# Kernel optimization log

Hardware: AMD Instinct MI355X
Metric: run time of the kernel (lower is better)

Reference implementation:

```python
import jax, jax.numpy as jnp
import numpy as np

NH = 8      # num_heads
KP = 3      # propagation_steps

def _ln(x, g, b, eps=1e-5):
    m = jnp.mean(x, -1, keepdims=True)
    v = jnp.mean(jnp.square(x - m), -1, keepdims=True)
    return (x - m) * jax.lax.rsqrt(v + eps) * g + b

def _mha(x, Wq, bq, Wk, bk, Wv, bv, Wo, bo):
    B, L, H = x.shape
    dh = H // NH
    q = (x @ Wq + bq).reshape(B, L, NH, dh)
    k = (x @ Wk + bk).reshape(B, L, NH, dh)
    v = (x @ Wv + bv).reshape(B, L, NH, dh)
    s = jnp.einsum('blhd,bmhd->bhlm', q, k) / jnp.sqrt(jnp.asarray(dh, x.dtype))
    p = jax.nn.softmax(s, axis=-1)
    o = jnp.einsum('bhlm,bmhd->blhd', p, v).reshape(B, L, H)
    return o @ Wo + bo

def setup_inputs():
    B, S, N, H = 2, 12, 800, 64
    keys = jax.random.split(jax.random.key(0), 64)
    it = iter(range(64))
    def nk():
        return keys[next(it)]
    def w(shape):
        return jax.random.normal(nk(), shape, jnp.float32) * 0.02
    p = {}
    p['x'] = jax.random.normal(nk(), (B, S, N, H), jnp.float32)
    # uniform weights scaled by 1/N (~row-normalized dense adjacency)
    p['adj'] = jax.random.uniform(nk(), (B, N, N), jnp.float32) / N
    p['W_gp'] = w((H, H)); p['b_gp'] = jnp.zeros((H,), jnp.float32)
    for sfx in ('s', 't'):
        for nm in ('Wq', 'Wk', 'Wv', 'Wo'):
            p[nm + '_' + sfx] = w((H, H))
        for nm in ('bq', 'bk', 'bv', 'bo'):
            p[nm + '_' + sfx] = jnp.zeros((H,), jnp.float32)
        p['g_' + sfx] = jnp.ones((H,), jnp.float32)
        p['be_' + sfx] = jnp.zeros((H,), jnp.float32)
    p['W1'] = w((H, 4 * H)); p['b1'] = jnp.zeros((4 * H,), jnp.float32)
    p['W2'] = w((4 * H, H)); p['b2'] = jnp.zeros((H,), jnp.float32)
    p['g1'] = jnp.ones((H,), jnp.float32); p['be1'] = jnp.zeros((H,), jnp.float32)
    p['g2'] = jnp.ones((H,), jnp.float32); p['be2'] = jnp.zeros((H,), jnp.float32)
    return p

def reference(x, adj, W_gp, b_gp,
              Wq_s, Wk_s, Wv_s, Wo_s, bq_s, bk_s, bv_s, bo_s, g_s, be_s,
              Wq_t, Wk_t, Wv_t, Wo_t, bq_t, bk_t, bv_t, bo_t, g_t, be_t,
              W1, b1, W2, b2, g1, be1, g2, be2):
    B, S, N, H = x.shape
    residual = x
    # accident-aware scaling (hidden_dim >= 6 path)
    acc = x[..., -2] * jnp.exp(-x[..., -1] / 60.0)
    xs = x * (1.0 + 0.3 * acc[..., None])
    # graph propagation: linear then K steps of relu(A @ h), vectorized over time
    h = xs @ W_gp + b_gp
    for _ in range(KP):
        h = jax.nn.relu(jnp.einsum('bnm,bsmh->bsnh', adj, h))
    prop = h + residual
    # spatial attention over nodes within each timestep
    xsa = prop.reshape(B * S, N, H)
    a = _mha(xsa, Wq_s, bq_s, Wk_s, bk_s, Wv_s, bv_s, Wo_s, bo_s)
    a = _ln(a + xsa, g_s, be_s).reshape(B, S, N, H)
    # temporal attention over timesteps per node
    xta = a.transpose(0, 2, 1, 3).reshape(B * N, S, H)
    t = _mha(xta, Wq_t, bq_t, Wk_t, bk_t, Wv_t, bv_t, Wo_t, bo_t)
    t = _ln(t + xta, g_t, be_t).reshape(B, N, S, H).transpose(0, 2, 1, 3)
    attn_out = t
    # pre-norm FFN with residual, post-norm output
    f = _ln(attn_out, g1, be1)
    f = jax.nn.relu(f @ W1 + b1) @ W2 + b2
    f = f + attn_out
    return _ln(f, g2, be2)
```

## Files before the change

### kernel.cpp

```cpp
#include <hip/hip_runtime.h>
#include <hip/hip_bf16.h>

#define NB 2
#define NS 12
#define NN 800
#define HEADS 8
#define DH 8
#define NBS (NB*NS)
#define NR (NB*NS*NN)

typedef __attribute__((ext_vector_type(4))) float f32x4;
typedef __attribute__((ext_vector_type(4))) short s16x4;
typedef __attribute__((ext_vector_type(8))) short s16x8;

static __device__ __forceinline__ unsigned short f2bf(float f) {
  union { float f; unsigned u; } v; v.f = f;
  unsigned r = (v.u + 0x7FFFu + ((v.u >> 16) & 1u)) >> 16;
  return (unsigned short)r;
}
static __device__ __forceinline__ float bf2f(unsigned short u) {
  union { unsigned u; float f; } v;
  v.u = ((unsigned)u) << 16;
  return v.f;
}
static __device__ __forceinline__ float fexp2(float x) {
  return __builtin_amdgcn_exp2f(x);
}
static __device__ __forceinline__ unsigned cvtpk_bf16(float a, float b) {
  unsigned r;
  asm("v_cvt_pk_bf16_f32 %0, %1, %2" : "=v"(r) : "v"(a), "v"(b));
  return r;
}

#define SC_LOG2 (0.35355339059327373f * 1.44269504088896f)

__global__ __launch_bounds__(256) void k_adjbf(const float* __restrict__ adj,
                                               unsigned short* __restrict__ o) {
  int i = blockIdx.x * 256 + threadIdx.x;
  if (i >= NB * NN * NN / 4) return;
  float4 a = *(const float4*)(adj + (size_t)i * 4);
  ushort4 r;
  r.x = f2bf(a.x); r.y = f2bf(a.y); r.z = f2bf(a.z); r.w = f2bf(a.w);
  *(ushort4*)(o + (size_t)i * 4) = r;
}

__global__ __launch_bounds__(256) void k_w2bf(
    const float* __restrict__ w0, const float* __restrict__ w1,
    const float* __restrict__ w2, const float* __restrict__ w3,
    const float* __restrict__ w4, const float* __restrict__ w5,
    const float* __restrict__ w6, const float* __restrict__ w7,
    const float* __restrict__ w8, unsigned short* __restrict__ out) {
  const float* ws[9] = {w0, w1, w2, w3, w4, w5, w6, w7, w8};
  int y = blockIdx.y;
  int i = blockIdx.x * 256 + threadIdx.x;
  if (i < 4096) out[y * 4096 + i] = f2bf(ws[y][i]);
}

__global__ __launch_bounds__(256) void k_f2bf(const float* __restrict__ src,
                                              unsigned short* __restrict__ dst,
                                              int n) {
  int i = blockIdx.x * 256 + threadIdx.x;
  if (i < n) dst[i] = f2bf(src[i]);
}

__global__ __launch_bounds__(256) void k_lin64T(
    const float* __restrict__ x, const unsigned short* __restrict__ Wb,
    const float* __restrict__ bias, unsigned short* __restrict__ HP) {
  __shared__ unsigned short As[32][36];
  __shared__ unsigned short Bs[64][36];
  const int tid = threadIdx.x;
  const int r0 = blockIdx.x * 32;
  const int w = tid >> 6, l = tid & 63;
  const int rb = (w & 1) * 16, cb = (w >> 1) * 32;
  f32x4 acc0 = {0.f, 0.f, 0.f, 0.f}, acc1 = {0.f, 0.f, 0.f, 0.f};
  const int ar = tid >> 3, ak = (tid & 7) * 4;
  const int bc = tid & 63, bm0 = (tid >> 6) * 4;
  const int k4 = (l >> 4) * 4;
  const int arow = rb + (l & 15);
  const int bcol0 = cb + (l & 15);
  const float* xrow = x + (size_t)(r0 + ar) * 64;
  float sf = 1.0f + 0.3f * xrow[62] * __expf(-xrow[63] * (1.0f / 60.0f));
  for (int k0 = 0; k0 < 64; k0 += 32) {
    __syncthreads();
    float4 xv = *(const float4*)(xrow + k0 + ak);
    ushort4 xb;
    xb.x = f2bf(xv.x * sf); xb.y = f2bf(xv.y * sf);
    xb.z = f2bf(xv.z * sf); xb.w = f2bf(xv.w * sf);
    *(ushort4*)&As[ar][ak] = xb;
#pragma unroll
    for (int j = 0; j < 4; ++j) {
      int mp = bm0 + j;
      unsigned lo = Wb[(size_t)(k0 + 2 * mp) * 64 + bc];
      unsigned hi = Wb[(size_t)(k0 + 2 * mp + 1) * 64 + bc];
      *(unsigned*)&Bs[bc][2 * mp] = lo | (hi << 16);
    }
    __syncthreads();
    s16x4 alo = *(const s16x4*)&As[arow][k4];
    s16x4 ahi = *(const s16x4*)&As[arow][k4 + 16];
    s16x8 a = {alo.x, alo.y, alo.z, alo.w, ahi.x, ahi.y, ahi.z, ahi.w};
    s16x4 b0l = *(const s16x4*)&Bs[bcol0][k4];
    s16x4 b0h = *(const s16x4*)&Bs[bcol0][k4 + 16];
    s16x8 bf0 = {b0l.x, b0l.y, b0l.z, b0l.w, b0h.x, b0h.y, b0h.z, b0h.w};
    s16x4 b1l = *(const s16x4*)&Bs[bcol0 + 16][k4];
    s16x4 b1h = *(const s16x4*)&Bs[bcol0 + 16][k4 + 16];
    s16x8 bf1 = {b1l.x, b1l.y, b1l.z, b1l.w, b1h.x, b1h.y, b1h.z, b1h.w};
    acc0 = __builtin_amdgcn_mfma_f32_16x16x32_bf16(a, bf0, acc0, 0, 0, 0);
    acc1 = __builtin_amdgcn_mfma_f32_16x16x32_bf16(a, bf1, acc1, 0, 0, 0);
  }
  const int c0 = cb + (l & 15);
  float b0 = bias[c0], b1 = bias[c0 + 16];
#pragma unroll
  for (int r = 0; r < 4; ++r) {
    int row = r0 + rb + (l >> 4) * 4 + r;
    int bs = row / NN, m = row % NN;
    HP[((size_t)bs * 64 + c0) * NN + m] = f2bf(acc0[r] + b0);
    HP[((size_t)bs * 64 + c0 + 16) * NN + m] = f2bf(acc1[r] + b1);
  }
}

template <bool LAST>
__global__ __launch_bounds__(256) void k_prop_mfma(
    const unsigned short* __restrict__ adjB,
    const unsigned short* __restrict__ HPin,
    const float* __restrict__ x,
    unsigned short* __restrict__ HPout,
    float* __restrict__ pout,
    unsigned short* __restrict__ pbout) {
  __shared__ unsigned short As[32][36];
  __shared__ unsigned short Bs[64][40];
  const int tid = threadIdx.x;
  const int bid = blockIdx.x;
  const int bs = bid / 25, mt = bid % 25;
  const int b = bs / NS;
  const int n0 = mt * 32;
  const unsigned short* abase = adjB + (size_t)b * NN * NN + (size_t)n0 * NN;
  const unsigned short* hbase = HPin + (size_t)bs * 64 * NN;
  const int w = tid >> 6, l = tid & 63;
  const int rb = (w & 1) * 16;
  const int cb = (w >> 1) * 32;
  f32x4 acc0 = {0.f, 0.f, 0.f, 0.f}, acc1 = {0.f, 0.f, 0.f, 0.f};
  const int ar = tid >> 3, ak = (tid & 7) * 4;
  const int bc = tid & 63, bq = tid >> 6;
  const int k4 = (l >> 4) * 4;
  const int arow = rb + (l & 15);
  const int bcol0 = cb + (l & 15);
  for (int m0 = 0; m0 < NN; m0 += 32) {
    __syncthreads();
    *(s16x4*)&As[ar][ak] = *(const s16x4*)(abase + (size_t)ar * NN + m0 + ak);
    *(s16x8*)&Bs[bc][bq * 8] =
        *(const s16x8*)(hbase + (size_t)bc * NN + m0 + bq * 8);
    __syncthreads();
    s16x4 alo = *(const s16x4*)&As[arow][k4];
    s16x4 ahi = *(const s16x4*)&As[arow][k4 + 16];
    s16x8 a = {alo.x, alo.y, alo.z, alo.w, ahi.x, ahi.y, ahi.z, ahi.w};
    s16x4 b0l = *(const s16x4*)&Bs[bcol0][k4];
    s16x4 b0h = *(const s16x4*)&Bs[bcol0][k4 + 16];
    s16x8 bf0 = {b0l.x, b0l.y, b0l.z, b0l.w, b0h.x, b0h.y, b0h.z, b0h.w};
    s16x4 b1l = *(const s16x4*)&Bs[bcol0 + 16][k4];
    s16x4 b1h = *(const s16x4*)&Bs[bcol0 + 16][k4 + 16];
    s16x8 bf1 = {b1l.x, b1l.y, b1l.z, b1l.w, b1h.x, b1h.y, b1h.z, b1h.w};
    acc0 = __builtin_amdgcn_mfma_f32_16x16x32_bf16(a, bf0, acc0, 0, 0, 0);
    acc1 = __builtin_amdgcn_mfma_f32_16x16x32_bf16(a, bf1, acc1, 0, 0, 0);
  }
  const int c0 = cb + (l & 15);
  if (LAST) {
#pragma unroll
    for (int r = 0; r < 4; ++r) {
      int n = n0 + rb + (l >> 4) * 4 + r;
      float v0 = fmaxf(acc0[r], 0.f);
      float v1 = fmaxf(acc1[r], 0.f);
      size_t i0 = ((size_t)bs * NN + n) * 64 + c0;
      size_t i1 = i0 + 16;
      float p0 = v0 + x[i0], p1 = v1 + x[i1];
      pout[i0] = p0;
      pout[i1] = p1;
      pbout[i0] = f2bf(p0);
      pbout[i1] = f2bf(p1);
    }
  } else {
    int nb = n0 + rb + (l >> 4) * 4;
    s16x4 o0, o1;
#pragma unroll
    for (int r = 0; r < 4; ++r) {
      o0[r] = (short)f2bf(fmaxf(acc0[r], 0.f));
      o1[r] = (short)f2bf(fmaxf(acc1[r], 0.f));
    }
    *(s16x4*)&HPout[((size_t)bs * 64 + c0) * NN + nb] = o0;
    *(s16x4*)&HPout[((size_t)bs * 64 + c0 + 16) * NN + nb] = o1;
  }
}

__global__ __launch_bounds__(256) void k_qkv_mfma(
    const unsigned short* __restrict__ Xb,
    const unsigned short* __restrict__ Wq,
    const unsigned short* __restrict__ Wk,
    const unsigned short* __restrict__ Wv,
    const float* __restrict__ bq, const float* __restrict__ bk,
    const float* __restrict__ bv, float qscale,
    unsigned short* __restrict__ Qo, unsigned short* __restrict__ Ko,
    unsigned short* __restrict__ Vo) {
  __shared__ unsigned short As[32][36];
  __shared__ unsigned short Bs[3][64][36];
  const int tid = threadIdx.x;
  const int r0 = blockIdx.x * 32;
  const int w = tid >> 6, l = tid & 63;
  const int rb = (w & 1) * 16;
  const int cb = (w >> 1) * 32;
  f32x4 acc[3][2];
#pragma unroll
  for (int i = 0; i < 3; ++i)
#pragma unroll
    for (int j = 0; j < 2; ++j) acc[i][j] = (f32x4){0.f, 0.f, 0.f, 0.f};
  const unsigned short* Wm[3] = {Wq, Wk, Wv};
  const int ar = tid >> 3, ak = (tid & 7) * 4;
  const int bc = tid & 63, bm0 = (tid >> 6) * 4;
  const int k4 = (l >> 4) * 4;
  const int arow = rb + (l & 15);
  const int bcol0 = cb + (l & 15);
  for (int k0 = 0; k0 < 64; k0 += 32) {
    __syncthreads();
    *(s16x4*)&As[ar][ak] =
        *(const s16x4*)(Xb + (size_t)(r0 + ar) * 64 + k0 + ak);
#pragma unroll
    for (int wm = 0; wm < 3; ++wm) {
#pragma unroll
      for (int j = 0; j < 4; ++j) {
        int mp = bm0 + j;
        unsigned lo = Wm[wm][(size_t)(k0 + 2 * mp) * 64 + bc];
        unsigned hi = Wm[wm][(size_t)(k0 + 2 * mp + 1) * 64 + bc];
        *(unsigned*)&Bs[wm][bc][2 * mp] = lo | (hi << 16);
      }
    }
    __syncthreads();
    s16x4 alo = *(const s16x4*)&As[arow][k4];
    s16x4 ahi = *(const s16x4*)&As[arow][k4 + 16];
    s16x8 a = {alo.x, alo.y, alo.z, alo.w, ahi.x, ahi.y, ahi.z, ahi.w};
#pragma unroll
    for (int wm = 0; wm < 3; ++wm) {
      s16x4 b0l = *(const s16x4*)&Bs[wm][bcol0][k4];
      s16x4 b0h = *(const s16x4*)&Bs[wm][bcol0][k4 + 16];
      s16x8 bf0 = {b0l.x, b0l.y, b0l.z, b0l.w, b0h.x, b0h.y, b0h.z, b0h.w};
      s16x4 b1l = *(const s16x4*)&Bs[wm][bcol0 + 16][k4];
      s16x4 b1h = *(const s16x4*)&Bs[wm][bcol0 + 16][k4 + 16];
      s16x8 bf1 = {b1l.x, b1l.y, b1l.z, b1l.w, b1h.x, b1h.y, b1h.z, b1h.w};
      acc[wm][0] = __builtin_amdgcn_mfma_f32_16x16x32_bf16(a, bf0, acc[wm][0], 0, 0, 0);
      acc[wm][1] = __builtin_amdgcn_mfma_f32_16x16x32_bf16(a, bf1, acc[wm][1], 0, 0, 0);
    }
  }
  const float* bm[3] = {bq, bk, bv};
  unsigned short* Om[3] = {Qo, Ko, Vo};
  const int c0 = cb + (l & 15);
#pragma unroll
  for (int wm = 0; wm < 3; ++wm) {
    float b0 = bm[wm][c0], b1 = bm[wm][c0 + 16];
    float sc = (wm == 0) ? qscale : 1.0f;
#pragma unroll
    for (int r = 0; r < 4; ++r) {
      int row = r0 + rb + (l >> 4) * 4 + r;
      Om[wm][(size_t)row * 64 + c0] = f2bf((acc[wm][0][r] + b0) * sc);
      Om[wm][(size_t)row * 64 + c0 + 16] = f2bf((acc[wm][1][r] + b1) * sc);
    }
  }
}

__global__ __launch_bounds__(256) void k_sattn4(
    const unsigned short* __restrict__ Qb,
    const unsigned short* __restrict__ Kb,
    const unsigned short* __restrict__ Vb,
    unsigned short* __restrict__ OB) {
  __shared__ unsigned short Ks[800][8];
  __shared__ unsigned short Vt[25 * 256 + 256];
  const int bs = blockIdx.x, h = blockIdx.y;
  const int tid = threadIdx.x;
  const size_t base = (size_t)bs * NN * 64 + h * DH;
  for (int r = tid; r < NN; r += 256)
    *(s16x8*)&Ks[r][0] = *(const s16x8*)(Kb + base + (size_t)r * 64);
  if (tid < 200) {
    int t = tid >> 3, c = tid & 7;
    int r = t * 32 + c * 4;
    s16x8 v0 = *(const s16x8*)(Vb + base + (size_t)r * 64);
    s16x8 v1 = *(const s16x8*)(Vb + base + (size_t)(r + 1) * 64);
    s16x8 v2 = *(const s16x8*)(Vb + base + (size_t)(r + 2) * 64);
    s16x8 v3 = *(const s16x8*)(Vb + base + (size_t)(r + 3) * 64);
#pragma unroll
    for (int d = 0; d < 8; ++d) {
      unsigned lo = (unsigned short)v0[d] | ((unsigned)(unsigned short)v1[d] << 16);
      unsigned hi = (unsigned short)v2[d] | ((unsigned)(unsigned short)v3[d] << 16);
      unsigned* dst = (unsigned*)&Vt[t * 256 + d * 32 + ((c ^ d) & 7) * 4];
      dst[0] = lo;
      dst[1] = hi;
    }
  }
  __syncthreads();
  const int w = tid >> 6, l = tid & 63;
  const int q0 = blockIdx.z * 128 + w * 32;
  if (q0 >= NN) return;
  const int r15 = l & 15, g = l >> 4;
  const int dd = r15;
  const int off1 = dd * 32 + ((g ^ dd) & 7) * 4;
  const int off2 = dd * 32 + (((4 + g) ^ dd) & 7) * 4;
  s16x4 qvA = *(const s16x4*)(Qb + base + (size_t)(q0 + r15) * 64 + (g & 1) * 4);
  s16x4 qvB = *(const s16x4*)(Qb + base + (size_t)(q0 + 16 + r15) * 64 + (g & 1) * 4);
  s16x8 qfA = {0, 0, 0, 0, 0, 0, 0, 0};
  s16x8 qfB = {0, 0, 0, 0, 0, 0, 0, 0};
  if (g < 2) {
    qfA[0] = qvA.x; qfA[1] = qvA.y; qfA[2] = qvA.z; qfA[3] = qvA.w;
    qfB[0] = qvB.x; qfB[1] = qvB.y; qfB[2] = qvB.z; qfB[3] = qvB.w;
  }
  const short one_bf = (short)0x3F80;
  f32x4 accA = {0.f, 0.f, 0.f, 0.f}, accB = {0.f, 0.f, 0.f, 0.f};
  const f32x4 zero4 = {0.f, 0.f, 0.f, 0.f};
  for (int t = 0; t < 25; ++t) {
    s16x4 ka = *(const s16x4*)&Ks[t * 32 + r15][(g & 1) * 4];
    s16x4 kb = *(const s16x4*)&Ks[t * 32 + 16 + r15][(g & 1) * 4];
    s16x8 kfa = {0, 0, 0, 0, 0, 0, 0, 0};
    s16x8 kfb = {0, 0, 0, 0, 0, 0, 0, 0};
    if (g < 2) {
      kfa[0] = ka.x; kfa[1] = ka.y; kfa[2] = ka.z; kfa[3] = ka.w;
      kfb[0] = kb.x; kfb[1] = kb.y; kfb[2] = kb.z; kfb[3] = kb.w;
    }
    s16x4 va = *(const s16x4*)&Vt[t * 256 + off1];
    s16x4 vb = *(const s16x4*)&Vt[t * 256 + off2];
    s16x8 vf;
    if (dd < 8) {
      vf = (s16x8){va.x, va.y, va.z, va.w, vb.x, vb.y, vb.z, vb.w};
    } else if (dd == 8) {
      vf = (s16x8){one_bf, one_bf, one_bf, one_bf, one_bf, one_bf, one_bf, one_bf};
    } else {
      vf = (s16x8){0, 0, 0, 0, 0, 0, 0, 0};
    }
    f32x4 sA1 = __builtin_amdgcn_mfma_f32_16x16x32_bf16(kfa, qfA, zero4, 0, 0, 0);
    f32x4 sA2 = __builtin_amdgcn_mfma_f32_16x16x32_bf16(kfb, qfA, zero4, 0, 0, 0);
    f32x4 sB1 = __builtin_amdgcn_mfma_f32_16x16x32_bf16(kfa, qfB, zero4, 0, 0, 0);
    f32x4 sB2 = __builtin_amdgcn_mfma_f32_16x16x32_bf16(kfb, qfB, zero4, 0, 0, 0);
    float pA[8], pB[8];
#pragma unroll
    for (int r = 0; r < 4; ++r) {
      pA[r] = fexp2(sA1[r]);
      pA[4 + r] = fexp2(sA2[r]);
      pB[r] = fexp2(sB1[r]);
      pB[4 + r] = fexp2(sB2[r]);
    }
    union { unsigned u[4]; s16x8 v; } puA, puB;
    puA.u[0] = cvtpk_bf16(pA[0], pA[1]);
    puA.u[1] = cvtpk_bf16(pA[2], pA[3]);
    puA.u[2] = cvtpk_bf16(pA[4], pA[5]);
    puA.u[3] = cvtpk_bf16(pA[6], pA[7]);
    puB.u[0] = cvtpk_bf16(pB[0], pB[1]);
    puB.u[1] = cvtpk_bf16(pB[2], pB[3]);
    puB.u[2] = cvtpk_bf16(pB[4], pB[5]);
    puB.u[3] = cvtpk_bf16(pB[6], pB[7]);
    accA = __builtin_amdgcn_mfma_f32_16x16x32_bf16(vf, puA.v, accA, 0, 0, 0);
    accB = __builtin_amdgcn_mfma_f32_16x16x32_bf16(vf, puB.v, accB, 0, 0, 0);
  }
  float lsA = __shfl(accA[0], 32 + r15, 64);
  float lsB = __shfl(accB[0], 32 + r15, 64);
  float invA = 1.f / lsA;
  float invB = 1.f / lsB;
  if (g < 2) {
#pragma unroll
    for (int r = 0; r < 4; ++r) {
      int d = g * 4 + r;
      OB[base + (size_t)(q0 + r15) * 64 + d] = f2bf(accA[r] * invA);
      OB[base + (size_t)(q0 + 16 + r15) * 64 + d] = f2bf(accB[r] * invB);
    }
  }
}

template <bool BF2>
__global__ __launch_bounds__(256) void k_projln_mfma(
    const unsigned short* __restrict__ Xb,
    const unsigned short* __restrict__ Wb,
    const float* __restrict__ bias, const float* __restrict__ res,
    const float* __restrict__ g, const float* __restrict__ be,
    float* __restrict__ out, unsigned short* __restrict__ bfout) {
  __shared__ unsigned short As[32][36];
  __shared__ unsigned short Bs[64][36];
  __shared__ float CT[32][68];
  const int tid = threadIdx.x;
  const int r0 = blockIdx.x * 32;
  const int w = tid >> 6, l = tid & 63;
  const int rb = (w & 1) * 16, cb = (w >> 1) * 32;
  f32x4 acc0 = {0.f, 0.f, 0.f, 0.f}, acc1 = {0.f, 0.f, 0.f, 0.f};
  const int ar = tid >> 3, ak = (tid & 7) * 4;
  const int bc = tid & 63, bm0 = (tid >> 6) * 4;
  const int k4 = (l >> 4) * 4;
  const int arow = rb + (l & 15);
  const int bcol0 = cb + (l & 15);
  for (int k0 = 0; k0 < 64; k0 += 32) {
    __syncthreads();
    *(s16x4*)&As[ar][ak] = *(const s16x4*)(Xb + (size_t)(r0 + ar) * 64 + k0 + ak);
#pragma unroll
    for (int j = 0; j < 4; ++j) {
      int mp = bm0 + j;
      unsigned lo = Wb[(size_t)(k0 + 2 * mp) * 64 + bc];
      unsigned hi = Wb[(size_t)(k0 + 2 * mp + 1) * 64 + bc];
      *(unsigned*)&Bs[bc][2 * mp] = lo | (hi << 16);
    }
    __syncthreads();
    s16x4 alo = *(const s16x4*)&As[arow][k4];
    s16x4 ahi = *(const s16x4*)&As[arow][k4 + 16];
    s16x8 a = {alo.x, alo.y, alo.z, alo.w, ahi.x, ahi.y, ahi.z, ahi.w};
    s16x4 b0l = *(const s16x4*)&Bs[bcol0][k4];
    s16x4 b0h = *(const s16x4*)&Bs[bcol0][k4 + 16];
    s16x8 bf0 = {b0l.x, b0l.y, b0l.z, b0l.w, b0h.x, b0h.y, b0h.z, b0h.w};
    s16x4 b1l = *(const s16x4*)&Bs[bcol0 + 16][k4];
    s16x4 b1h = *(const s16x4*)&Bs[bcol0 + 16][k4 + 16];
    s16x8 bf1 = {b1l.x, b1l.y, b1l.z, b1l.w, b1h.x, b1h.y, b1h.z, b1h.w};
    acc0 = __builtin_amdgcn_mfma_f32_16x16x32_bf16(a, bf0, acc0, 0, 0, 0);
    acc1 = __builtin_amdgcn_mfma_f32_16x16x32_bf16(a, bf1, acc1, 0, 0, 0);
  }
  const int c0 = cb + (l & 15);
#pragma unroll
  for (int r = 0; r < 4; ++r) {
    int row = rb + (l >> 4) * 4 + r;
    size_t gi = (size_t)(r0 + row) * 64;
    CT[row][c0] = acc0[r] + bias[c0] + res[gi + c0];
    CT[row][c0 + 16] = acc1[r] + bias[c0 + 16] + res[gi + c0 + 16];
  }
  __syncthreads();
  const int row = tid >> 3, sub = tid & 7;
  float v[8];
#pragma unroll
  for (int i = 0; i < 8; ++i) v[i] = CT[row][sub * 8 + i];
  float s = 0.f;
#pragma unroll
  for (int i = 0; i < 8; ++i) s += v[i];
#pragma unroll
  for (int off = 1; off < 8; off <<= 1) s += __shfl_xor(s, off, 64);
  float mean = s * (1.f / 64.f);
  float q = 0.f;
#pragma unroll
  for (int i = 0; i < 8; ++i) {
    float ddd = v[i] - mean;
    q += ddd * ddd;
  }
#pragma unroll
  for (int off = 1; off < 8; off <<= 1) q += __shfl_xor(q, off, 64);
  float rstd = rsqrtf(q * (1.f / 64.f) + 1e-5f);
  float r4[8];
#pragma unroll
  for (int i = 0; i < 8; ++i)
    r4[i] = (v[i] - mean) * rstd * g[sub * 8 + i] + be[sub * 8 + i];
  float* op = out + (size_t)(r0 + row) * 64 + sub * 8;
  *(float4*)op = (float4){r4[0], r4[1], r4[2], r4[3]};
  *(float4*)(op + 4) = (float4){r4[4], r4[5], r4[6], r4[7]};
  if (BF2) {
    unsigned short* bp = bfout + (size_t)(r0 + row) * 64 + sub * 8;
#pragma unroll
    for (int i = 0; i < 8; ++i) bp[i] = f2bf(r4[i]);
  }
}

__global__ __launch_bounds__(256) void k_tattn(
    const unsigned short* __restrict__ Q, const unsigned short* __restrict__ K,
    const unsigned short* __restrict__ V, unsigned short* __restrict__ O) {
  int b = blockIdx.x / NN, n = blockIdx.x % NN;
  __shared__ float Qs[12][64], Ks[12][64], Vs[12][64];
  int tid = threadIdx.x;
  for (int i = tid; i < 12 * 64; i += 256) {
    int s = i >> 6, c = i & 63;
    size_t idx = (((size_t)b * NS + s) * NN + n) * 64 + c;
    Qs[s][c] = bf2f(Q[idx]);
    Ks[s][c] = bf2f(K[idx]);
    Vs[s][c] = bf2f(V[idx]);
  }
  __syncthreads();
  for (int wi = tid; wi < 12 * 64; wi += 256) {
    int l = wi >> 6, c = wi & 63;
    int h8 = c & 56;
    float sc[12];
    float mx = -1e30f;
#pragma unroll
    for (int m = 0; m < 12; ++m) {
      float s = 0.f;
#pragma unroll
      for (int d = 0; d < 8; ++d) s += Qs[l][h8 + d] * Ks[m][h8 + d];
      s *= 0.35355339059327373f;
      sc[m] = s;
      mx = fmaxf(mx, s);
    }
    float sum = 0.f;
#pragma unroll
    for (int m = 0; m < 12; ++m) {
      sc[m] = __expf(sc[m] - mx);
      sum += sc[m];
    }
    float inv = 1.f / sum;
    float o = 0.f;
#pragma unroll
    for (int m = 0; m < 12; ++m) o += sc[m] * Vs[m][c];
    size_t idx = (((size_t)b * NS + l) * NN + n) * 64 + c;
    O[idx] = f2bf(o * inv);
  }
}

__global__ __launch_bounds__(256) void k_ln(const float* __restrict__ X,
                                            const float* __restrict__ g,
                                            const float* __restrict__ be,
                                            unsigned short* __restrict__ out) {
  int tid = threadIdx.x;
  int lane = tid & 63, w = tid >> 6;
  int row = blockIdx.x * 4 + w;
  float acc = X[(size_t)row * 64 + lane];
  float s = acc;
#pragma unroll
  for (int off = 32; off; off >>= 1) s += __shfl_xor(s, off, 64);
  float mean = s * (1.f / 64.f);
  float d = acc - mean;
  float v = d * d;
#pragma unroll
  for (int off = 32; off; off >>= 1) v += __shfl_xor(v, off, 64);
  float rstd = rsqrtf(v * (1.f / 64.f) + 1e-5f);
  out[(size_t)row * 64 + lane] = f2bf(d * rstd * g[lane] + be[lane]);
}

__global__ __launch_bounds__(256) void k_ffn1_mfma(
    const unsigned short* __restrict__ Xb,
    const unsigned short* __restrict__ W1b,
    const float* __restrict__ b1, unsigned short* __restrict__ Hid) {
  __shared__ unsigned short As[32][36];
  __shared__ unsigned short Bs[64][36];
  const int tid = threadIdx.x;
  const int r0 = blockIdx.x * 32;
  const int n0 = blockIdx.y * 64;
  const int w = tid >> 6, l = tid & 63;
  const int rb = (w & 1) * 16, cb = (w >> 1) * 32;
  f32x4 acc0 = {0.f, 0.f, 0.f, 0.f}, acc1 = {0.f, 0.f, 0.f, 0.f};
  const int ar = tid >> 3, ak = (tid & 7) * 4;
  const int bc = tid & 63, bm0 = (tid >> 6) * 4;
  const int k4 = (l >> 4) * 4;
  const int arow = rb + (l & 15);
  const int bcol0 = cb + (l & 15);
  for (int k0 = 0; k0 < 64; k0 += 32) {
    __syncthreads();
    *(s16x4*)&As[ar][ak] = *(const s16x4*)(Xb + (size_t)(r0 + ar) * 64 + k0 + ak);
#pragma unroll
    for (int j = 0; j < 4; ++j) {
      int mp = bm0 + j;
      unsigned lo = W1b[(size_t)(k0 + 2 * mp) * 256 + n0 + bc];
      unsigned hi = W1b[(size_t)(k0 + 2 * mp + 1) * 256 + n0 + bc];
      *(unsigned*)&Bs[bc][2 * mp] = lo | (hi << 16);
    }
    __syncthreads();
    s16x4 alo = *(const s16x4*)&As[arow][k4];
    s16x4 ahi = *(const s16x4*)&As[arow][k4 + 16];
    s16x8 a = {alo.x, alo.y, alo.z, alo.w, ahi.x, ahi.y, ahi.z, ahi.w};
    s16x4 b0l = *(const s16x4*)&Bs[bcol0][k4];
    s16x4 b0h = *(const s16x4*)&Bs[bcol0][k4 + 16];
    s16x8 bf0 = {b0l.x, b0l.y, b0l.z, b0l.w, b0h.x, b0h.y, b0h.z, b0h.w};
    s16x4 b1l = *(const s16x4*)&Bs[bcol0 + 16][k4];
    s16x4 b1h = *(const s16x4*)&Bs[bcol0 + 16][k4 + 16];
    s16x8 bf1 = {b1l.x, b1l.y, b1l.z, b1l.w, b1h.x, b1h.y, b1h.z, b1h.w};
    acc0 = __builtin_amdgcn_mfma_f32_16x16x32_bf16(a, bf0, acc0, 0, 0, 0);
    acc1 = __builtin_amdgcn_mfma_f32_16x16x32_bf16(a, bf1, acc1, 0, 0, 0);
  }
  const int c0 = cb + (l & 15);
  float b0 = b1[n0 + c0], bb1 = b1[n0 + c0 + 16];
#pragma unroll
  for (int r = 0; r < 4; ++r) {
    int row = r0 + rb + (l >> 4) * 4 + r;
    Hid[(size_t)row * 256 + n0 + c0] = f2bf(fmaxf(acc0[r] + b0, 0.f));
    Hid[(size_t)row * 256 + n0 + c0 + 16] = f2bf(fmaxf(acc1[r] + bb1, 0.f));
  }
}

__global__ __launch_bounds__(256) void k_ffn2ln_mfma(
    const unsigned short* __restrict__ Hd,
    const unsigned short* __restrict__ W2b,
    const float* __restrict__ b2, const float* __restrict__ res,
    const float* __restrict__ g, const float* __restrict__ be,
    float* __restrict__ out) {
  __shared__ unsigned short As[32][36];
  __shared__ unsigned short Bs[64][36];
  __shared__ float CT[32][68];
  const int tid = threadIdx.x;
  const int r0 = blockIdx.x * 32;
  const int w = tid >> 6, l = tid & 63;
  const int rb = (w & 1) * 16, cb = (w >> 1) * 32;
  f32x4 acc0 = {0.f, 0.f, 0.f, 0.f}, acc1 = {0.f, 0.f, 0.f, 0.f};
  const int ar = tid >> 3, ak = (tid & 7) * 4;
  const int bc = tid & 63, bm0 = (tid >> 6) * 4;
  const int k4 = (l >> 4) * 4;
  const int arow = rb + (l & 15);
  const int bcol0 = cb + (l & 15);
  for (int k0 = 0; k0 < 256; k0 += 32) {
    __syncthreads();
    *(s16x4*)&As[ar][ak] = *(const s16x4*)(Hd + (size_t)(r0 + ar) * 256 + k0 + ak);
#pragma unroll
    for (int j = 0; j < 4; ++j) {
      int mp = bm0 + j;
      unsigned lo = W2b[(size_t)(k0 + 2 * mp) * 64 + bc];
      unsigned hi = W2b[(size_t)(k0 + 2 * mp + 1) * 64 + bc];
      *(unsigned*)&Bs[bc][2 * mp] = lo | (hi << 16);
    }
    __syncthreads();
    s16x4 alo = *(const s16x4*)&As[arow][k4];
    s16x4 ahi = *(const s16x4*)&As[arow][k4 + 16];
    s16x8 a = {alo.x, alo.y, alo.z, alo.w, ahi.x, ahi.y, ahi.z, ahi.w};
    s16x4 b0l = *(const s16x4*)&Bs[bcol0][k4];
    s16x4 b0h = *(const s16x4*)&Bs[bcol0][k4 + 16];
    s16x8 bf0 = {b0l.x, b0l.y, b0l.z, b0l.w, b0h.x, b0h.y, b0h.z, b0h.w};
    s16x4 b1l = *(const s16x4*)&Bs[bcol0 + 16][k4];
    s16x4 b1h = *(const s16x4*)&Bs[bcol0 + 16][k4 + 16];
    s16x8 bf1 = {b1l.x, b1l.y, b1l.z, b1l.w, b1h.x, b1h.y, b1h.z, b1h.w};
    acc0 = __builtin_amdgcn_mfma_f32_16x16x32_bf16(a, bf0, acc0, 0, 0, 0);
    acc1 = __builtin_amdgcn_mfma_f32_16x16x32_bf16(a, bf1, acc1, 0, 0, 0);
  }
  const int c0 = cb + (l & 15);
#pragma unroll
  for (int r = 0; r < 4; ++r) {
    int row = rb + (l >> 4) * 4 + r;
    size_t gi = (size_t)(r0 + row) * 64;
    CT[row][c0] = acc0[r] + b2[c0] + res[gi + c0];
    CT[row][c0 + 16] = acc1[r] + b2[c0 + 16] + res[gi + c0 + 16];
  }
  __syncthreads();
  const int row = tid >> 3, sub = tid & 7;
  float v[8];
#pragma unroll
  for (int i = 0; i < 8; ++i) v[i] = CT[row][sub * 8 + i];
  float s = 0.f;
#pragma unroll
  for (int i = 0; i < 8; ++i) s += v[i];
#pragma unroll
  for (int off = 1; off < 8; off <<= 1) s += __shfl_xor(s, off, 64);
  float mean = s * (1.f / 64.f);
  float q = 0.f;
#pragma unroll
  for (int i = 0; i < 8; ++i) {
    float d = v[i] - mean;
    q += d * d;
  }
#pragma unroll
  for (int off = 1; off < 8; off <<= 1) q += __shfl_xor(q, off, 64);
  float rstd = rsqrtf(q * (1.f / 64.f) + 1e-5f);
  float r4[8];
#pragma unroll
  for (int i = 0; i < 8; ++i)
    r4[i] = (v[i] - mean) * rstd * g[sub * 8 + i] + be[sub * 8 + i];
  float* op = out + (size_t)(r0 + row) * 64 + sub * 8;
  *(float4*)op = (float4){r4[0], r4[1], r4[2], r4[3]};
  *(float4*)(op + 4) = (float4){r4[4], r4[5], r4[6], r4[7]};
}

extern "C" void kernel_launch(void* const* d_in, const int* in_sizes, int n_in,
                              void* d_out, int out_size, void* d_ws,
                              size_t ws_size, hipStream_t stream) {
  const float* x = (const float*)d_in[0];
  const float* adj = (const float*)d_in[1];
  const float* W_gp = (const float*)d_in[2];
  const float* b_gp = (const float*)d_in[3];
  const float* Wq_s = (const float*)d_in[4];
  const float* Wk_s = (const float*)d_in[5];
  const float* Wv_s = (const float*)d_in[6];
  const float* Wo_s = (const float*)d_in[7];
  const float* bq_s = (const float*)d_in[8];
  const float* bk_s = (const float*)d_in[9];
  const float* bv_s = (const float*)d_in[10];
  const float* bo_s = (const float*)d_in[11];
  const float* g_s = (const float*)d_in[12];
  const float* be_s = (const float*)d_in[13];
  const float* Wq_t = (const float*)d_in[14];
  const float* Wk_t = (const float*)d_in[15];
  const float* Wv_t = (const float*)d_in[16];
  const float* Wo_t = (const float*)d_in[17];
  const float* bq_t = (const float*)d_in[18];
  const float* bk_t = (const float*)d_in[19];
  const float* bv_t = (const float*)d_in[20];
  const float* bo_t = (const float*)d_in[21];
  const float* g_t = (const float*)d_in[22];
  const float* be_t = (const float*)d_in[23];
  const float* W1 = (const float*)d_in[24];
  const float* b1 = (const float*)d_in[25];
  const float* W2 = (const float*)d_in[26];
  const float* b2 = (const float*)d_in[27];
  const float* g1 = (const float*)d_in[28];
  const float* be1 = (const float*)d_in[29];
  const float* g2 = (const float*)d_in[30];
  const float* be2 = (const float*)d_in[31];
  float* out = (float*)d_out;

  float* ws = (float*)d_ws;
  const size_t U = (size_t)NR * 64;
  float* A = ws + 0 * U;
  float* Bb = ws + 1 * U;
  float* C = ws + 2 * U;
  float* D = ws + 3 * U;
  float* P = ws + 4 * U;
  unsigned short* QB = (unsigned short*)A;
  unsigned short* KB = (unsigned short*)Bb;
  unsigned short* VB = (unsigned short*)C;
  unsigned short* OBuf = (unsigned short*)D;
  unsigned short* Q2 = (unsigned short*)Bb;
  unsigned short* K2 = (unsigned short*)C;
  unsigned short* V2 = (unsigned short*)D;
  unsigned short* PB = (unsigned short*)(ws + 5 * U);
  unsigned short* HIDB = (unsigned short*)(ws + 5 * U);
  unsigned short* LNB = (unsigned short*)(ws + 7 * U);
  unsigned short* TB = LNB;
  unsigned short* W1B = (unsigned short*)(ws + 7 * U + U / 2);
  unsigned short* W2B = W1B + 16384;
  unsigned short* HP0 = (unsigned short*)(ws + 9 * U);
  unsigned short* HP1 = (unsigned short*)(ws + 9 * U + U / 2);
  unsigned short* ADJB = (unsigned short*)(ws + 10 * U);
  unsigned short* WB = (unsigned short*)(ws + 10 * U + 650240);

  dim3 blk(256);
  k_w2bf<<<dim3(16, 9), blk, 0, stream>>>(Wq_s, Wk_s, Wv_s, Wq_t, Wk_t, Wv_t,
                                          W_gp, Wo_s, Wo_t, WB);
  k_f2bf<<<64, blk, 0, stream>>>(W1, W1B, 16384);
  k_f2bf<<<64, blk, 0, stream>>>(W2, W2B, 16384);
  k_adjbf<<<(NB * NN * NN / 4 + 255) / 256, blk, 0, stream>>>(adj, ADJB);
  k_lin64T<<<NR / 32, blk, 0, stream>>>(x, WB + 6 * 4096, b_gp, HP0);
  k_prop_mfma<false><<<NBS * 25, blk, 0, stream>>>(ADJB, HP0, x, HP1, P, PB);
  k_prop_mfma<false><<<NBS * 25, blk, 0, stream>>>(ADJB, HP1, x, HP0, P, PB);
  k_prop_mfma<true><<<NBS * 25, blk, 0, stream>>>(ADJB, HP0, x, HP1, P, PB);
  k_qkv_mfma<<<NR / 32, blk, 0, stream>>>(PB, WB, WB + 4096, WB + 8192, bq_s,
                                          bk_s, bv_s, SC_LOG2, QB, KB, VB);
  k_sattn4<<<dim3(NBS, HEADS, 7), blk, 0, stream>>>(QB, KB, VB, OBuf);
  k_projln_mfma<true><<<NR / 32, blk, 0, stream>>>(OBuf, WB + 7 * 4096, bo_s, P,
                                                   g_s, be_s, A, PB);
  k_qkv_mfma<<<NR / 32, blk, 0, stream>>>(PB, WB + 12288, WB + 16384,
                                          WB + 20480, bq_t, bk_t, bv_t, 1.0f,
                                          Q2, K2, V2);
  k_tattn<<<NB * NN, blk, 0, stream>>>(Q2, K2, V2, TB);
  k_projln_mfma<false><<<NR / 32, blk, 0, stream>>>(
      TB, WB + 8 * 4096, bo_t, A, g_t, be_t, Bb, (unsigned short*)nullptr);
  k_ln<<<NR / 4, blk, 0, stream>>>(Bb, g1, be1, LNB);
  k_ffn1_mfma<<<dim3(NR / 32, 4), blk, 0, stream>>>(LNB, W1B, b1, HIDB);
  k_ffn2ln_mfma<<<NR / 32, blk, 0, stream>>>(HIDB, W2B, b2, Bb, g2, be2, out);
}
```

Measured before the change: 155.1 us.

## Fuse FFN halves, fold pre-FFN LayerNorm into projection, convert adjacency inline

Merges the three weight-conversion kernels into one launch. The adjacency bf16 conversion pass is dropped, and each propagation step converts fp32 adjacency tiles while loading them. The standalone LayerNorm kernel is folded into the temporal output projection epilogue. The two FFN GEMMs are fused so the 256-wide hidden activation stays in shared memory instead of going through global memory. In exchange, adjacency is read as fp32 three times and converted repeatedly, and the fused FFN uses more shared memory per block.

New measurement: 158.3 us. 2.0% more time.

```diff
diff --git a/kernel.cpp b/kernel.cpp
--- a/kernel.cpp
+++ b/kernel.cpp
@@ -34,33 +34,23 @@
 
 #define SC_LOG2 (0.35355339059327373f * 1.44269504088896f)
 
-__global__ __launch_bounds__(256) void k_adjbf(const float* __restrict__ adj,
-                                               unsigned short* __restrict__ o) {
-  int i = blockIdx.x * 256 + threadIdx.x;
-  if (i >= NB * NN * NN / 4) return;
-  float4 a = *(const float4*)(adj + (size_t)i * 4);
-  ushort4 r;
-  r.x = f2bf(a.x); r.y = f2bf(a.y); r.z = f2bf(a.z); r.w = f2bf(a.w);
-  *(ushort4*)(o + (size_t)i * 4) = r;
-}
-
-__global__ __launch_bounds__(256) void k_w2bf(
+__global__ __launch_bounds__(256) void k_wconv(
     const float* __restrict__ w0, const float* __restrict__ w1,
     const float* __restrict__ w2, const float* __restrict__ w3,
     const float* __restrict__ w4, const float* __restrict__ w5,
     const float* __restrict__ w6, const float* __restrict__ w7,
-    const float* __restrict__ w8, unsigned short* __restrict__ out) {
-  const float* ws[9] = {w0, w1, w2, w3, w4, w5, w6, w7, w8};
-  int y = blockIdx.y;
+    const float* __restrict__ w8, const float* __restrict__ W1,
+    const float* __restrict__ W2, unsigned short* __restrict__ WB,
+    unsigned short* __restrict__ W1B, unsigned short* __restrict__ W2B) {
   int i = blockIdx.x * 256 + threadIdx.x;
-  if (i < 4096) out[y * 4096 + i] = f2bf(ws[y][i]);
-}
-
-__global__ __launch_bounds__(256) void k_f2bf(const float* __restrict__ src,
-                                              unsigned short* __restrict__ dst,
-                                              int n) {
-  int i = blockIdx.x * 256 + threadIdx.x;
-  if (i < n) dst[i] = f2bf(src[i]);
+  if (i < 36864) {
+    const float* ws[9] = {w0, w1, w2, w3, w4, w5, w6, w7, w8};
+    WB[i] = f2bf(ws[i >> 12][i & 4095]);
+  } else if (i < 53248) {
+    W1B[i - 36864] = f2bf(W1[i - 36864]);
+  } else if (i < 69632) {
+    W2B[i - 53248] = f2bf(W2[i - 53248]);
+  }
 }
 
 __global__ __launch_bounds__(256) void k_lin64T(
@@ -120,7 +110,7 @@
 
 template <bool LAST>
 __global__ __launch_bounds__(256) void k_prop_mfma(
-    const unsigned short* __restrict__ adjB,
+    const float* __restrict__ adj,
     const unsigned short* __restrict__ HPin,
     const float* __restrict__ x,
     unsigned short* __restrict__ HPout,
@@ -133,7 +123,7 @@
   const int bs = bid / 25, mt = bid % 25;
   const int b = bs / NS;
   const int n0 = mt * 32;
-  const unsigned short* abase = adjB + (size_t)b * NN * NN + (size_t)n0 * NN;
+  const float* abase = adj + (size_t)b * NN * NN + (size_t)n0 * NN;
   const unsigned short* hbase = HPin + (size_t)bs * 64 * NN;
   const int w = tid >> 6, l = tid & 63;
   const int rb = (w & 1) * 16;
@@ -146,7 +136,11 @@
   const int bcol0 = cb + (l & 15);
   for (int m0 = 0; m0 < NN; m0 += 32) {
     __syncthreads();
-    *(s16x4*)&As[ar][ak] = *(const s16x4*)(abase + (size_t)ar * NN + m0 + ak);
+    float4 av = *(const float4*)(abase + (size_t)ar * NN + m0 + ak);
+    ushort4 ab;
+    ab.x = f2bf(av.x); ab.y = f2bf(av.y);
+    ab.z = f2bf(av.z); ab.w = f2bf(av.w);
+    *(ushort4*)&As[ar][ak] = ab;
     *(s16x8*)&Bs[bc][bq * 8] =
         *(const s16x8*)(hbase + (size_t)bc * NN + m0 + bq * 8);
     __syncthreads();
@@ -367,12 +361,13 @@
   }
 }
 
-template <bool BF2>
+template <bool LN2>
 __global__ __launch_bounds__(256) void k_projln_mfma(
     const unsigned short* __restrict__ Xb,
     const unsigned short* __restrict__ Wb,
     const float* __restrict__ bias, const float* __restrict__ res,
     const float* __restrict__ g, const float* __restrict__ be,
+    const float* __restrict__ g2, const float* __restrict__ be2,
     float* __restrict__ out, unsigned short* __restrict__ bfout) {
   __shared__ unsigned short As[32][36];
   __shared__ unsigned short Bs[64][36];
@@ -445,10 +440,29 @@
   float* op = out + (size_t)(r0 + row) * 64 + sub * 8;
   *(float4*)op = (float4){r4[0], r4[1], r4[2], r4[3]};
   *(float4*)(op + 4) = (float4){r4[4], r4[5], r4[6], r4[7]};
-  if (BF2) {
-    unsigned short* bp = bfout + (size_t)(r0 + row) * 64 + sub * 8;
+  unsigned short* bp = bfout + (size_t)(r0 + row) * 64 + sub * 8;
+  if (!LN2) {
 #pragma unroll
     for (int i = 0; i < 8; ++i) bp[i] = f2bf(r4[i]);
+  } else {
+    float s2 = 0.f;
+#pragma unroll
+    for (int i = 0; i < 8; ++i) s2 += r4[i];
+#pragma unroll
+    for (int off = 1; off < 8; off <<= 1) s2 += __shfl_xor(s2, off, 64);
+    float mean2 = s2 * (1.f / 64.f);
+    float q2 = 0.f;
+#pragma unroll
+    for (int i = 0; i < 8; ++i) {
+      float d2 = r4[i] - mean2;
+      q2 += d2 * d2;
+    }
+#pragma unroll
+    for (int off = 1; off < 8; off <<= 1) q2 += __shfl_xor(q2, off, 64);
+    float rstd2 = rsqrtf(q2 * (1.f / 64.f) + 1e-5f);
+#pragma unroll
+    for (int i = 0; i < 8; ++i)
+      bp[i] = f2bf((r4[i] - mean2) * rstd2 * g2[sub * 8 + i] + be2[sub * 8 + i]);
   }
 }
 
@@ -495,56 +509,84 @@
   }
 }
 
-__global__ __launch_bounds__(256) void k_ln(const float* __restrict__ X,
-                                            const float* __restrict__ g,
-                                            const float* __restrict__ be,
-                                            unsigned short* __restrict__ out) {
-  int tid = threadIdx.x;
-  int lane = tid & 63, w = tid >> 6;
-  int row = blockIdx.x * 4 + w;
-  float acc = X[(size_t)row * 64 + lane];
-  float s = acc;
-#pragma unroll
-  for (int off = 32; off; off >>= 1) s += __shfl_xor(s, off, 64);
-  float mean = s * (1.f / 64.f);
-  float d = acc - mean;
-  float v = d * d;
-#pragma unroll
-  for (int off = 32; off; off >>= 1) v += __shfl_xor(v, off, 64);
-  float rstd = rsqrtf(v * (1.f / 64.f) + 1e-5f);
-  out[(size_t)row * 64 + lane] = f2bf(d * rstd * g[lane] + be[lane]);
-}
-
-__global__ __launch_bounds__(256) void k_ffn1_mfma(
+__global__ __launch_bounds__(256) void k_ffn_fused(
     const unsigned short* __restrict__ Xb,
     const unsigned short* __restrict__ W1b,
-    const float* __restrict__ b1, unsigned short* __restrict__ Hid) {
-  __shared__ unsigned short As[32][36];
-  __shared__ unsigned short Bs[64][36];
+    const float* __restrict__ b1,
+    const unsigned short* __restrict__ W2b,
+    const float* __restrict__ b2,
+    const float* __restrict__ res,
+    const float* __restrict__ g, const float* __restrict__ be,
+    float* __restrict__ out) {
+  __shared__ unsigned short As[32][68];
+  __shared__ unsigned short Bs[64][66];
+  __shared__ unsigned short Hs[32][264];
+  __shared__ float CT[32][68];
   const int tid = threadIdx.x;
   const int r0 = blockIdx.x * 32;
-  const int n0 = blockIdx.y * 64;
   const int w = tid >> 6, l = tid & 63;
   const int rb = (w & 1) * 16, cb = (w >> 1) * 32;
+  const int r15 = l & 15;
+  const int k4 = (l >> 4) * 4;
+  const int arow = rb + r15;
+  const int bcol0 = cb + r15;
+  {
+    int ar = tid >> 3, ak8 = (tid & 7) * 8;
+    *(s16x8*)&As[ar][ak8] = *(const s16x8*)(Xb + (size_t)(r0 + ar) * 64 + ak8);
+  }
+  const int sbc = tid & 63;
+  for (int c = 0; c < 4; ++c) {
+    __syncthreads();
+    {
+      const int smp0 = (tid >> 6) * 8;
+      int gcol = c * 64 + sbc;
+#pragma unroll
+      for (int j = 0; j < 8; ++j) {
+        int mp = smp0 + j;
+        unsigned lo = W1b[(size_t)(2 * mp) * 256 + gcol];
+        unsigned hi = W1b[(size_t)(2 * mp + 1) * 256 + gcol];
+        *(unsigned*)&Bs[sbc][2 * mp] = lo | (hi << 16);
+      }
+    }
+    __syncthreads();
+    f32x4 acc0 = {0.f, 0.f, 0.f, 0.f}, acc1 = {0.f, 0.f, 0.f, 0.f};
+#pragma unroll
+    for (int k0 = 0; k0 < 64; k0 += 32) {
+      s16x4 alo = *(const s16x4*)&As[arow][k0 + k4];
+      s16x4 ahi = *(const s16x4*)&As[arow][k0 + k4 + 16];
+      s16x8 a = {alo.x, alo.y, alo.z, alo.w, ahi.x, ahi.y, ahi.z, ahi.w};
+      s16x4 b0l = *(const s16x4*)&Bs[bcol0][k0 + k4];
+      s16x4 b0h = *(const s16x4*)&Bs[bcol0][k0 + k4 + 16];
+      s16x8 bf0 = {b0l.x, b0l.y, b0l.z, b0l.w, b0h.x, b0h.y, b0h.z, b0h.w};
+      s16x4 b1l = *(const s16x4*)&Bs[bcol0 + 16][k0 + k4];
+      s16x4 b1h = *(const s16x4*)&Bs[bcol0 + 16][k0 + k4 + 16];
+      s16x8 bf1 = {b1l.x, b1l.y, b1l.z, b1l.w, b1h.x, b1h.y, b1h.z, b1h.w};
+      acc0 = __builtin_amdgcn_mfma_f32_16x16x32_bf16(a, bf0, acc0, 0, 0, 0);
+      acc1 = __builtin_amdgcn_mfma_f32_16x16x32_bf16(a, bf1, acc1, 0, 0, 0);
+    }
+    int c0 = cb + r15;
+    float bb0 = b1[c * 64 + c0], bb1v = b1[c * 64 + c0 + 16];
+#pragma unroll
+    for (int r = 0; r < 4; ++r) {
+      int row = rb + (l >> 4) * 4 + r;
+      Hs[row][c * 64 + c0] = f2bf(fmaxf(acc0[r] + bb0, 0.f));
+      Hs[row][c * 64 + c0 + 16] = f2bf(fmaxf(acc1[r] + bb1v, 0.f));
+    }
+  }
   f32x4 acc0 = {0.f, 0.f, 0.f, 0.f}, acc1 = {0.f, 0.f, 0.f, 0.f};
-  const int ar = tid >> 3, ak = (tid & 7) * 4;
-  const int bc = tid & 63, bm0 = (tid >> 6) * 4;
-  const int k4 = (l >> 4) * 4;
-  const int arow = rb + (l & 15);
-  const int bcol0 = cb + (l & 15);
-  for (int k0 = 0; k0 < 64; k0 += 32) {
-    __syncthreads();
-    *(s16x4*)&As[ar][ak] = *(const s16x4*)(Xb + (size_t)(r0 + ar) * 64 + k0 + ak);
+  const int smp4 = (tid >> 6) * 4;
+  for (int k0 = 0; k0 < 256; k0 += 32) {
+    __syncthreads();
 #pragma unroll
     for (int j = 0; j < 4; ++j) {
-      int mp = bm0 + j;
-      unsigned lo = W1b[(size_t)(k0 + 2 * mp) * 256 + n0 + bc];
-      unsigned hi = W1b[(size_t)(k0 + 2 * mp + 1) * 256 + n0 + bc];
-      *(unsigned*)&Bs[bc][2 * mp] = lo | (hi << 16);
-    }
-    __syncthreads();
-    s16x4 alo = *(const s16x4*)&As[arow][k4];
-    s16x4 ahi = *(const s16x4*)&As[arow][k4 + 16];
+      int mp = smp4 + j;
+      unsigned lo = W2b[(size_t)(k0 + 2 * mp) * 64 + sbc];
+      unsigned hi = W2b[(size_t)(k0 + 2 * mp + 1) * 64 + sbc];
+      *(unsigned*)&Bs[sbc][2 * mp] = lo | (hi << 16);
+    }
+    __syncthreads();
+    s16x4 alo = *(const s16x4*)&Hs[arow][k0 + k4];
+    s16x4 ahi = *(const s16x4*)&Hs[arow][k0 + k4 + 16];
     s16x8 a = {alo.x, alo.y, alo.z, alo.w, ahi.x, ahi.y, ahi.z, ahi.w};
     s16x4 b0l = *(const s16x4*)&Bs[bcol0][k4];
     s16x4 b0h = *(const s16x4*)&Bs[bcol0][k4 + 16];
@@ -555,59 +597,7 @@
     acc0 = __builtin_amdgcn_mfma_f32_16x16x32_bf16(a, bf0, acc0, 0, 0, 0);
     acc1 = __builtin_amdgcn_mfma_f32_16x16x32_bf16(a, bf1, acc1, 0, 0, 0);
   }
-  const int c0 = cb + (l & 15);
-  float b0 = b1[n0 + c0], bb1 = b1[n0 + c0 + 16];
-#pragma unroll
-  for (int r = 0; r < 4; ++r) {
-    int row = r0 + rb + (l >> 4) * 4 + r;
-    Hid[(size_t)row * 256 + n0 + c0] = f2bf(fmaxf(acc0[r] + b0, 0.f));
-    Hid[(size_t)row * 256 + n0 + c0 + 16] = f2bf(fmaxf(acc1[r] + bb1, 0.f));
-  }
-}
-
-__global__ __launch_bounds__(256) void k_ffn2ln_mfma(
-    const unsigned short* __restrict__ Hd,
-    const unsigned short* __restrict__ W2b,
-    const float* __restrict__ b2, const float* __restrict__ res,
-    const float* __restrict__ g, const float* __restrict__ be,
-    float* __restrict__ out) {
-  __shared__ unsigned short As[32][36];
-  __shared__ unsigned short Bs[64][36];
-  __shared__ float CT[32][68];
-  const int tid = threadIdx.x;
-  const int r0 = blockIdx.x * 32;
-  const int w = tid >> 6, l = tid & 63;
-  const int rb = (w & 1) * 16, cb = (w >> 1) * 32;
-  f32x4 acc0 = {0.f, 0.f, 0.f, 0.f}, acc1 = {0.f, 0.f, 0.f, 0.f};
-  const int ar = tid >> 3, ak = (tid & 7) * 4;
-  const int bc = tid & 63, bm0 = (tid >> 6) * 4;
-  const int k4 = (l >> 4) * 4;
-  const int arow = rb + (l & 15);
-  const int bcol0 = cb + (l & 15);
-  for (int k0 = 0; k0 < 256; k0 += 32) {
-    __syncthreads();
-    *(s16x4*)&As[ar][ak] = *(const s16x4*)(Hd + (size_t)(r0 + ar) * 256 + k0 + ak);
-#pragma unroll
-    for (int j = 0; j < 4; ++j) {
-      int mp = bm0 + j;
-      unsigned lo = W2b[(size_t)(k0 + 2 * mp) * 64 + bc];
-      unsigned hi = W2b[(size_t)(k0 + 2 * mp + 1) * 64 + bc];
-      *(unsigned*)&Bs[bc][2 * mp] = lo | (hi << 16);
-    }
-    __syncthreads();
-    s16x4 alo = *(const s16x4*)&As[arow][k4];
-    s16x4 ahi = *(const s16x4*)&As[arow][k4 + 16];
-    s16x8 a = {alo.x, alo.y, alo.z, alo.w, ahi.x, ahi.y, ahi.z, ahi.w};
-    s16x4 b0l = *(const s16x4*)&Bs[bcol0][k4];
-    s16x4 b0h = *(const s16x4*)&Bs[bcol0][k4 + 16];
-    s16x8 bf0 = {b0l.x, b0l.y, b0l.z, b0l.w, b0h.x, b0h.y, b0h.z, b0h.w};
-    s16x4 b1l = *(const s16x4*)&Bs[bcol0 + 16][k4];
-    s16x4 b1h = *(const s16x4*)&Bs[bcol0 + 16][k4 + 16];
-    s16x8 bf1 = {b1l.x, b1l.y, b1l.z, b1l.w, b1h.x, b1h.y, b1h.z, b1h.w};
-    acc0 = __builtin_amdgcn_mfma_f32_16x16x32_bf16(a, bf0, acc0, 0, 0, 0);
-    acc1 = __builtin_amdgcn_mfma_f32_16x16x32_bf16(a, bf1, acc1, 0, 0, 0);
-  }
-  const int c0 = cb + (l & 15);
+  const int c0 = cb + r15;
 #pragma unroll
   for (int r = 0; r < 4; ++r) {
     int row = rb + (l >> 4) * 4 + r;
@@ -692,42 +682,36 @@
   unsigned short* KB = (unsigned short*)Bb;
   unsigned short* VB = (unsigned short*)C;
   unsigned short* OBuf = (unsigned short*)D;
-  unsigned short* Q2 = (unsigned short*)Bb;
-  unsigned short* K2 = (unsigned short*)C;
-  unsigned short* V2 = (unsigned short*)D;
+  unsigned short* Q2 = (unsigned short*)C;
+  unsigned short* K2 = (unsigned short*)D;
+  unsigned short* V2 = (unsigned short*)(ws + 5 * U + U);
   unsigned short* PB = (unsigned short*)(ws + 5 * U);
-  unsigned short* HIDB = (unsigned short*)(ws + 5 * U);
   unsigned short* LNB = (unsigned short*)(ws + 7 * U);
   unsigned short* TB = LNB;
   unsigned short* W1B = (unsigned short*)(ws + 7 * U + U / 2);
   unsigned short* W2B = W1B + 16384;
   unsigned short* HP0 = (unsigned short*)(ws + 9 * U);
   unsigned short* HP1 = (unsigned short*)(ws + 9 * U + U / 2);
-  unsigned short* ADJB = (unsigned short*)(ws + 10 * U);
   unsigned short* WB = (unsigned short*)(ws + 10 * U + 650240);
 
   dim3 blk(256);
-  k_w2bf<<<dim3(16, 9), blk, 0, stream>>>(Wq_s, Wk_s, Wv_s, Wq_t, Wk_t, Wv_t,
-                                          W_gp, Wo_s, Wo_t, WB);
-  k_f2bf<<<64, blk, 0, stream>>>(W1, W1B, 16384);
-  k_f2bf<<<64, blk, 0, stream>>>(W2, W2B, 16384);
-  k_adjbf<<<(NB * NN * NN / 4 + 255) / 256, blk, 0, stream>>>(adj, ADJB);
+  k_wconv<<<272, blk, 0, stream>>>(Wq_s, Wk_s, Wv_s, Wq_t, Wk_t, Wv_t, W_gp,
+                                   Wo_s, Wo_t, W1, W2, WB, W1B, W2B);
   k_lin64T<<<NR / 32, blk, 0, stream>>>(x, WB + 6 * 4096, b_gp, HP0);
-  k_prop_mfma<false><<<NBS * 25, blk, 0, stream>>>(ADJB, HP0, x, HP1, P, PB);
-  k_prop_mfma<false><<<NBS * 25, blk, 0, stream>>>(ADJB, HP1, x, HP0, P, PB);
-  k_prop_mfma<true><<<NBS * 25, blk, 0, stream>>>(ADJB, HP0, x, HP1, P, PB);
+  k_prop_mfma<false><<<NBS * 25, blk, 0, stream>>>(adj, HP0, x, HP1, P, PB);
+  k_prop_mfma<false><<<NBS * 25, blk, 0, stream>>>(adj, HP1, x, HP0, P, PB);
+  k_prop_mfma<true><<<NBS * 25, blk, 0, stream>>>(adj, HP0, x, HP1, P, PB);
   k_qkv_mfma<<<NR / 32, blk, 0, stream>>>(PB, WB, WB + 4096, WB + 8192, bq_s,
                                           bk_s, bv_s, SC_LOG2, QB, KB, VB);
   k_sattn4<<<dim3(NBS, HEADS, 7), blk, 0, stream>>>(QB, KB, VB, OBuf);
-  k_projln_mfma<true><<<NR / 32, blk, 0, stream>>>(OBuf, WB + 7 * 4096, bo_s, P,
-                                                   g_s, be_s, A, PB);
+  k_projln_mfma<false><<<NR / 32, blk, 0, stream>>>(
+      OBuf, WB + 7 * 4096, bo_s, P, g_s, be_s, nullptr, nullptr, A, PB);
   k_qkv_mfma<<<NR / 32, blk, 0, stream>>>(PB, WB + 12288, WB + 16384,
                                           WB + 20480, bq_t, bk_t, bv_t, 1.0f,
                                           Q2, K2, V2);
   k_tattn<<<NB * NN, blk, 0, stream>>>(Q2, K2, V2, TB);
-  k_projln_mfma<false><<<NR / 32, blk, 0, stream>>>(
-      TB, WB + 8 * 4096, bo_t, A, g_t, be_t, Bb, (unsigned short*)nullptr);
-  k_ln<<<NR / 4, blk, 0, stream>>>(Bb, g1, be1, LNB);
-  k_ffn1_mfma<<<dim3(NR / 32, 4), blk, 0, stream>>>(LNB, W1B, b1, HIDB);
-  k_ffn2ln_mfma<<<NR / 32, blk, 0, stream>>>(HIDB, W2B, b2, Bb, g2, be2, out);
-}
+  k_projln_mfma<true><<<NR / 32, blk, 0, stream>>>(
+      TB, WB + 8 * 4096, bo_t, A, g_t, be_t, g1, be1, Bb, LNB);
+  k_ffn_fused<<<NR / 32, blk, 0, stream>>>(LNB, W1B, b1, W2B, b2, Bb, g2, be2,
+                                           out);
+}
```
